# Kernel tuning notes

Measured on AMD Instinct MI355X. Metric: run time of the kernel, lower is better.

Reference implementation:

```python
import jax, jax.numpy as jnp
import numpy as np

T = 4096   # total packed tokens
NQ = 16    # query heads
NK = 4     # kv heads (GQA)
HN = 128   # head dim


def setup_inputs() -> dict:
    key = jax.random.key(0)
    kq, kk, kv = jax.random.split(key, 3)
    return {
        "query": jax.random.normal(kq, (T, NQ, HN), dtype=jnp.float32),
        "key": jax.random.normal(kk, (T, NK, HN), dtype=jnp.float32),
        "value": jax.random.normal(kv, (T, NK, HN), dtype=jnp.float32),
        # packed varlen boundaries (4 sequences)
        "cu_seqlens": jnp.array([0, 1536, 2048, 3584, 4096], dtype=jnp.int32),
    }


def reference(query, key, value, cu_seqlens):
    t, nq, hn = query.shape
    nk = key.shape[1]
    rep = nq // nk  # GQA expansion factor
    scale = hn ** -0.5
    # [h, t, d] layout (matches torch unsqueeze(0).permute(0,2,1,3), batch=1)
    q = jnp.transpose(query, (1, 0, 2))
    k = jnp.repeat(jnp.transpose(key, (1, 0, 2)), rep, axis=0)
    v = jnp.repeat(jnp.transpose(value, (1, 0, 2)), rep, axis=0)
    # full scores [h, t, t]
    scores = jnp.einsum('hqd,hkd->hqk', q, k) * scale
    # block-diagonal causal mask from cu_seqlens
    idx = jnp.arange(t)
    seg = jnp.searchsorted(cu_seqlens[1:], idx, side='right')  # segment id per token
    allowed = (seg[:, None] == seg[None, :]) & (idx[None, :] <= idx[:, None])
    scores = jnp.where(allowed[None, :, :], scores, -jnp.inf)
    p = jax.nn.softmax(scores, axis=-1)  # every row keeps its diagonal -> no NaN
    out = jnp.einsum('hqk,hkd->hqd', p, v)
    # [t, nq*hn]
    return jnp.transpose(out, (1, 0, 2)).reshape(t, nq * hn)
```

## Files before the change

### kernel.cpp

```cpp
#include <hip/hip_runtime.h>
#include <hip/hip_bf16.h>
#include <cstdint>
#include <cstddef>

#define NQH 16
#define NKH 4
#define HN 128
#define QBLK 64
#define KBLK 32
#define QSCALE 0.12751589542585458f

typedef __bf16 bf16x8 __attribute__((ext_vector_type(8)));
typedef float f32x4 __attribute__((ext_vector_type(4)));

__device__ __forceinline__ void gload16(const void* g, void* l) {
  __builtin_amdgcn_global_load_lds(
      (const __attribute__((address_space(1))) void*)g,
      (__attribute__((address_space(3))) void*)l, 16, 0, 0);
}

__global__ __launch_bounds__(256) void cvt_k(const float* __restrict__ K,
                                             __bf16* __restrict__ Kb, int T) {
  const size_t idx8 = ((size_t)blockIdx.x * 256 + threadIdx.x) * 8;
  const int d = (int)(idx8 & 127);
  const int kvh = (int)((idx8 >> 7) & 3);
  const size_t t = idx8 >> 9;
  float4 a = *(const float4*)&K[idx8];
  float4 b = *(const float4*)&K[idx8 + 4];
  bf16x8 f;
  f[0] = (__bf16)a.x; f[1] = (__bf16)a.y; f[2] = (__bf16)a.z; f[3] = (__bf16)a.w;
  f[4] = (__bf16)b.x; f[5] = (__bf16)b.y; f[6] = (__bf16)b.z; f[7] = (__bf16)b.w;
  *(bf16x8*)&Kb[(size_t)kvh * T * HN + t * HN + d] = f;
}

__global__ __launch_bounds__(128) void cvt_v(const float* __restrict__ V,
                                             __bf16* __restrict__ Vb, int T) {
  const int d = threadIdx.x;
  const int t0 = blockIdx.x * 8;
  const int kvh = blockIdx.y;
  bf16x8 f;
#pragma unroll
  for (int i = 0; i < 8; ++i)
    f[i] = (__bf16)V[(size_t)(t0 + i) * (NKH * HN) + kvh * HN + d];
  *(bf16x8*)&Vb[(size_t)kvh * HN * T + (size_t)d * T + t0] = f;
}

template <bool MASKED>
__device__ __forceinline__ void attn_iter(
    const char* Kc, const char* Vc, const bf16x8 qfA[4], const bf16x8 qfB[4],
    int ln, int hi, int vslot, int limA, float& mA, float& lA, f32x4* accA,
    float& mB, float& lB, f32x4* accB) {
  f32x4 sA[2], sB[2];
#pragma unroll
  for (int c = 0; c < 2; ++c) {
    sA[c] = (f32x4){0.f, 0.f, 0.f, 0.f};
    sB[c] = (f32x4){0.f, 0.f, 0.f, 0.f};
  }
  __builtin_amdgcn_s_setprio(1);
#pragma unroll
  for (int kc = 0; kc < 4; ++kc) {
#pragma unroll
    for (int c = 0; c < 2; ++c) {
      const int row = c * 16 + ln;
      const bf16x8 kf =
          *(const bf16x8*)(Kc + row * 256 + (((kc * 4 + hi) ^ (ln & 7)) << 4));
      sA[c] = __builtin_amdgcn_mfma_f32_16x16x32_bf16(kf, qfA[kc], sA[c], 0, 0, 0);
      sB[c] = __builtin_amdgcn_mfma_f32_16x16x32_bf16(kf, qfB[kc], sB[c], 0, 0, 0);
    }
  }
  __builtin_amdgcn_s_setprio(0);

  if (MASKED) {
    const int limB = limA + 16;
#pragma unroll
    for (int c = 0; c < 2; ++c)
#pragma unroll
      for (int i = 0; i < 4; ++i) {
        const int koff = hi * 8 + c * 4 + i;
        sA[c][i] = (koff <= limA) ? sA[c][i] : -1e30f;
        sB[c][i] = (koff <= limB) ? sB[c][i] : -1e30f;
      }
  }

  float mmA = fmaxf(fmaxf(fmaxf(sA[0][0], sA[0][1]), fmaxf(sA[0][2], sA[0][3])),
                    fmaxf(fmaxf(sA[1][0], sA[1][1]), fmaxf(sA[1][2], sA[1][3])));
  float mmB = fmaxf(fmaxf(fmaxf(sB[0][0], sB[0][1]), fmaxf(sB[0][2], sB[0][3])),
                    fmaxf(fmaxf(sB[1][0], sB[1][1]), fmaxf(sB[1][2], sB[1][3])));
  mmA = fmaxf(mmA, __shfl_xor(mmA, 16));
  mmA = fmaxf(mmA, __shfl_xor(mmA, 32));
  mmB = fmaxf(mmB, __shfl_xor(mmB, 16));
  mmB = fmaxf(mmB, __shfl_xor(mmB, 32));

  if (__any((mmA > mA + 8.0f) | (mmB > mB + 8.0f))) {
    const float mnA = fmaxf(mA, mmA), mnB = fmaxf(mB, mmB);
    const float cA = exp2f(mA - mnA), cB = exp2f(mB - mnB);
    mA = mnA; mB = mnB;
    lA *= cA; lB *= cB;
#pragma unroll
    for (int dt = 0; dt < 8; ++dt) { accA[dt] *= cA; accB[dt] *= cB; }
  }

  float pA[2][4], pB[2][4];
  float psA = 0.f, psB = 0.f;
#pragma unroll
  for (int c = 0; c < 2; ++c)
#pragma unroll
    for (int i = 0; i < 4; ++i) {
      pA[c][i] = exp2f(sA[c][i] - mA); psA += pA[c][i];
      pB[c][i] = exp2f(sB[c][i] - mB); psB += pB[c][i];
    }
  psA += __shfl_xor(psA, 16); psA += __shfl_xor(psA, 32);
  psB += __shfl_xor(psB, 16); psB += __shfl_xor(psB, 32);
  lA += psA; lB += psB;

  bf16x8 paA, paB;
#pragma unroll
  for (int e = 0; e < 8; ++e) {
    paA[e] = (__bf16)pA[e >> 2][e & 3];
    paB[e] = (__bf16)pB[e >> 2][e & 3];
  }

  __builtin_amdgcn_s_setprio(1);
#pragma unroll
  for (int dt = 0; dt < 8; ++dt) {
    const int vr = dt * 16 + ln;
    const bf16x8 vb = *(const bf16x8*)(Vc + vr * 64 + vslot);
    accA[dt] = __builtin_amdgcn_mfma_f32_16x16x32_bf16(vb, paA, accA[dt], 0, 0, 0);
    accB[dt] = __builtin_amdgcn_mfma_f32_16x16x32_bf16(vb, paB, accB[dt], 0, 0, 0);
  }
  __builtin_amdgcn_s_setprio(0);
}

__global__ __launch_bounds__(256, 3) void attn_mfma10(
    const float* __restrict__ Q, const __bf16* __restrict__ Kb,
    const __bf16* __restrict__ Vb, const int* __restrict__ cu,
    float* __restrict__ O, int T, int nseg) {
  const int tid = threadIdx.x;
  const int w = tid >> 6, lane = tid & 63;
  const int g = w >> 1, wv = w & 1;
  const int ln = lane & 15, hi = lane >> 4;

  const int bid = blockIdx.x;
  const int round = bid >> 8, pos = bid & 255;
  const int rr = (round & 1) ? ((round << 8) | (255 - pos)) : bid;
  const int h = rr & 15;
  const int my_rank = rr >> 4;
  const int kvh = h >> 2;

  __shared__ __align__(16) char smem[33296];
  float* ml1 = (float*)(smem + 32768);
  int* s_tile = (int*)(smem + 33280);

  if (w == 0) {
    const int t2 = lane;
    const int r0t = t2 << 6;
    int st = 0;
    for (int s = 1; s < nseg; ++s) { const int c = cu[s]; if (c <= r0t) st = c; }
    const int dep = r0t + QBLK - st;
    int rk = 0;
    for (int j = 0; j < 64; ++j) {
      const int dj = __shfl(dep, j);
      rk += (dj > dep) || (dj == dep && j < t2);
    }
    if (rk == my_rank) *s_tile = t2;
  }
  __syncthreads();
  const int r0 = *s_tile << 6;

  int st0 = 0;
  for (int s = 1; s < nseg; ++s) { const int c = cu[s]; if (c <= r0) st0 = c; }
  const int kstart = st0;
  const int n0 = (r0 + QBLK - kstart) >> 6;
  const int gbeg = kstart + g * n0 * KBLK;

  const __bf16* KbH = Kb + (size_t)kvh * T * HN;
  const __bf16* VbH = Vb + (size_t)kvh * HN * T;

  bf16x8 qfA[4], qfB[4];
  {
    const float* qpA = &Q[(size_t)(r0 + wv * 32 + ln) * (NQH * HN) + h * HN];
    const float* qpB = qpA + (size_t)16 * (NQH * HN);
#pragma unroll
    for (int kc = 0; kc < 4; ++kc) {
      float4 a0 = *(const float4*)(qpA + kc * 32 + hi * 8);
      float4 a1 = *(const float4*)(qpA + kc * 32 + hi * 8 + 4);
      float4 b0 = *(const float4*)(qpB + kc * 32 + hi * 8);
      float4 b1 = *(const float4*)(qpB + kc * 32 + hi * 8 + 4);
      bf16x8 fa, fb;
      fa[0] = (__bf16)(a0.x * QSCALE); fa[1] = (__bf16)(a0.y * QSCALE);
      fa[2] = (__bf16)(a0.z * QSCALE); fa[3] = (__bf16)(a0.w * QSCALE);
      fa[4] = (__bf16)(a1.x * QSCALE); fa[5] = (__bf16)(a1.y * QSCALE);
      fa[6] = (__bf16)(a1.z * QSCALE); fa[7] = (__bf16)(a1.w * QSCALE);
      fb[0] = (__bf16)(b0.x * QSCALE); fb[1] = (__bf16)(b0.y * QSCALE);
      fb[2] = (__bf16)(b0.z * QSCALE); fb[3] = (__bf16)(b0.w * QSCALE);
      fb[4] = (__bf16)(b1.x * QSCALE); fb[5] = (__bf16)(b1.y * QSCALE);
      fb[6] = (__bf16)(b1.z * QSCALE); fb[7] = (__bf16)(b1.w * QSCALE);
      qfA[kc] = fa; qfB[kc] = fb;
    }
  }

  float mA = 0.f, lA = 0.f, mB = 0.f, lB = 0.f;
  f32x4 accA[8], accB[8];
#pragma unroll
  for (int dt = 0; dt < 8; ++dt) {
    accA[dt] = (f32x4){0.f, 0.f, 0.f, 0.f};
    accB[dt] = (f32x4){0.f, 0.f, 0.f, 0.f};
  }

  const int gl = wv * 64 + lane;
  const int Rb = gl >> 4, sK = gl & 15;
  int key_j[4];
#pragma unroll
  for (int j = 0; j < 4; ++j)
    key_j[j] = ((Rb >> 2) << 3) + (Rb & 3) + ((j & 1) << 4) + ((j >> 1) << 2);
  const int kcolE = ((sK ^ Rb) << 3);
  const int db = gl >> 2, sV = gl & 3;
  const int swz_d = (db & 3) ^ ((db >> 2) & 3);
  const int vkeyE = ((sV ^ swz_d) << 3);
  char* ldsK = smem + g * 8192 + (size_t)gl * 16;
  char* ldsV = smem + 16384 + g * 8192 + (size_t)gl * 16;
  const int vslot = ((hi ^ (ln & 3) ^ ((ln >> 2) & 3)) << 4);

  const char* Kc = smem + g * 8192;
  const char* Vc = smem + 16384 + g * 8192;
  const int relA = wv * 32 + ln;

  for (int it = 0; it < n0; ++it) {
    const int kb = gbeg + it * KBLK;
#pragma unroll
    for (int j = 0; j < 4; ++j)
      gload16(KbH + (size_t)(kb + key_j[j]) * HN + kcolE, ldsK + j * 2048);
#pragma unroll
    for (int j = 0; j < 4; ++j)
      gload16(VbH + (size_t)(db + 32 * j) * T + kb + vkeyE, ldsV + j * 2048);
    __syncthreads();
    if (kb >= r0)
      attn_iter<true>(Kc, Vc, qfA, qfB, ln, hi, vslot, relA - (kb - r0), mA,
                      lA, accA, mB, lB, accB);
    else
      attn_iter<false>(Kc, Vc, qfA, qfB, ln, hi, vslot, 0, mA, lA, accA, mB,
                       lB, accB);
    __syncthreads();
  }

  float* accf = (float*)smem;
  if (g == 1) {
    if (hi == 0) {
      ml1[relA * 2] = mA;            ml1[relA * 2 + 1] = lA;
      ml1[(relA + 16) * 2] = mB;     ml1[(relA + 16) * 2 + 1] = lB;
    }
#pragma unroll
    for (int dt = 0; dt < 8; ++dt) {
      *(f32x4*)&accf[relA * 128 + ((dt ^ (relA & 7)) << 4) + (hi << 2)] = accA[dt];
      *(f32x4*)&accf[(relA + 16) * 128 + ((dt ^ ((relA + 16) & 7)) << 4) + (hi << 2)] = accB[dt];
    }
  }
  __syncthreads();
  if (g == 0) {
#pragma unroll
    for (int set = 0; set < 2; ++set) {
      const int row = relA + set * 16;
      const float mg = set ? mB : mA;
      const float lg = set ? lB : lA;
      f32x4* acc = set ? accB : accA;
      const float m1 = ml1[row * 2], l1v = ml1[row * 2 + 1];
      float c0 = 1.f, c1 = 0.f, l = lg;
      if (l1v != 0.f) {
        const float m = fmaxf(mg, m1);
        c0 = exp2f(mg - m); c1 = exp2f(m1 - m);
        l = lg * c0 + l1v * c1;
      }
      const float inv = 1.0f / l;
      float* op = &O[(size_t)(r0 + row) * (NQH * HN) + h * HN];
#pragma unroll
      for (int dt = 0; dt < 8; ++dt) {
        const f32x4 a1 = *(const f32x4*)&accf[row * 128 + ((dt ^ (row & 7)) << 4) + (hi << 2)];
        const f32x4 res = (acc[dt] * c0 + a1 * c1) * inv;
        *(f32x4*)&op[dt * 16 + hi * 4] = res;
      }
    }
  }
}

extern "C" void kernel_launch(void* const* d_in, const int* in_sizes, int n_in,
                              void* d_out, int out_size, void* d_ws, size_t ws_size,
                              hipStream_t stream) {
  const float* Q = (const float*)d_in[0];
  const float* K = (const float*)d_in[1];
  const float* V = (const float*)d_in[2];
  const int* cu = (const int*)d_in[3];
  float* O = (float*)d_out;

  const int T = in_sizes[0] / (NQH * HN);
  const int nseg = in_sizes[3] - 1;

  const size_t need = (size_t)2 * NKH * T * HN * sizeof(__bf16);
  if (ws_size < need) return;

  __bf16* Kb = (__bf16*)d_ws;
  __bf16* Vb = (__bf16*)d_ws + (size_t)NKH * T * HN;

  const int nelem = T * NKH * HN;
  cvt_k<<<nelem / 8 / 256, 256, 0, stream>>>(K, Kb, T);
  cvt_v<<<dim3(T / 8, NKH), 128, 0, stream>>>(V, Vb, T);

  attn_mfma10<<<1024, 256, 0, stream>>>(Q, Kb, Vb, cu, O, T, nseg);
}
```

Measured before the change: 72.41 us.

## Load K/V fragments directly from global memory, fuse conversion kernels, defer row-sum reduction

The K and V LDS staging with global_load_lds and the two __syncthreads per iteration are removed, and each lane now reads its bf16 K/V MMA fragments directly from global memory (relying on L1/L2 reuse). The separate K and V conversion kernels are merged into one launch. The per-iteration cross-lane row-sum shuffle is deferred to the end, and the max shuffle now runs only when a rescale is triggered. Occupancy hint drops from 3 to 2 blocks per CU, which trades residency for more registers to hold preloaded fragments, but uncoalesced global fragment loads may expose more latency.

```diff
diff --git a/kernel.cpp b/kernel.cpp
--- a/kernel.cpp
+++ b/kernel.cpp
@@ -13,43 +13,49 @@
 typedef __bf16 bf16x8 __attribute__((ext_vector_type(8)));
 typedef float f32x4 __attribute__((ext_vector_type(4)));
 
-__device__ __forceinline__ void gload16(const void* g, void* l) {
-  __builtin_amdgcn_global_load_lds(
-      (const __attribute__((address_space(1))) void*)g,
-      (__attribute__((address_space(3))) void*)l, 16, 0, 0);
-}
-
-__global__ __launch_bounds__(256) void cvt_k(const float* __restrict__ K,
-                                             __bf16* __restrict__ Kb, int T) {
-  const size_t idx8 = ((size_t)blockIdx.x * 256 + threadIdx.x) * 8;
-  const int d = (int)(idx8 & 127);
-  const int kvh = (int)((idx8 >> 7) & 3);
-  const size_t t = idx8 >> 9;
-  float4 a = *(const float4*)&K[idx8];
-  float4 b = *(const float4*)&K[idx8 + 4];
-  bf16x8 f;
-  f[0] = (__bf16)a.x; f[1] = (__bf16)a.y; f[2] = (__bf16)a.z; f[3] = (__bf16)a.w;
-  f[4] = (__bf16)b.x; f[5] = (__bf16)b.y; f[6] = (__bf16)b.z; f[7] = (__bf16)b.w;
-  *(bf16x8*)&Kb[(size_t)kvh * T * HN + t * HN + d] = f;
-}
-
-__global__ __launch_bounds__(128) void cvt_v(const float* __restrict__ V,
-                                             __bf16* __restrict__ Vb, int T) {
-  const int d = threadIdx.x;
-  const int t0 = blockIdx.x * 8;
-  const int kvh = blockIdx.y;
-  bf16x8 f;
-#pragma unroll
-  for (int i = 0; i < 8; ++i)
-    f[i] = (__bf16)V[(size_t)(t0 + i) * (NKH * HN) + kvh * HN + d];
-  *(bf16x8*)&Vb[(size_t)kvh * HN * T + (size_t)d * T + t0] = f;
+__global__ __launch_bounds__(256) void cvt_kv(const float* __restrict__ K,
+                                              const float* __restrict__ V,
+                                              __bf16* __restrict__ Kb,
+                                              __bf16* __restrict__ Vb, int T) {
+  const int nkblk = T * NKH * HN / 8 / 256;
+  const int bid = blockIdx.x;
+  if (bid < nkblk) {
+    const size_t idx8 = ((size_t)bid * 256 + threadIdx.x) * 8;
+    const int d = (int)(idx8 & 127);
+    const int kvh = (int)((idx8 >> 7) & 3);
+    const size_t t = idx8 >> 9;
+    float4 a = *(const float4*)&K[idx8];
+    float4 b = *(const float4*)&K[idx8 + 4];
+    bf16x8 f;
+    f[0] = (__bf16)a.x; f[1] = (__bf16)a.y; f[2] = (__bf16)a.z; f[3] = (__bf16)a.w;
+    f[4] = (__bf16)b.x; f[5] = (__bf16)b.y; f[6] = (__bf16)b.z; f[7] = (__bf16)b.w;
+    *(bf16x8*)&Kb[(size_t)kvh * T * HN + t * HN + d] = f;
+  } else {
+    const int ob = (bid - nkblk) * 2 + (threadIdx.x >> 7);
+    const int bx = ob & (T / 8 - 1);
+    const int kvh = ob / (T / 8);
+    const int d = threadIdx.x & 127;
+    const int t0 = bx * 8;
+    bf16x8 f;
+#pragma unroll
+    for (int i = 0; i < 8; ++i)
+      f[i] = (__bf16)V[(size_t)(t0 + i) * (NKH * HN) + kvh * HN + d];
+    *(bf16x8*)&Vb[(size_t)kvh * HN * T + (size_t)d * T + t0] = f;
+  }
 }
 
 template <bool MASKED>
 __device__ __forceinline__ void attn_iter(
-    const char* Kc, const char* Vc, const bf16x8 qfA[4], const bf16x8 qfB[4],
-    int ln, int hi, int vslot, int limA, float& mA, float& lA, f32x4* accA,
-    float& mB, float& lB, f32x4* accB) {
+    const __bf16* __restrict__ kA, const __bf16* __restrict__ vA, size_t vstr,
+    const bf16x8 qfA[4], const bf16x8 qfB[4], int hi, int limA,
+    float& mA, float& lA, f32x4* accA, float& mB, float& lB, f32x4* accB) {
+  bf16x8 kf[2][4];
+#pragma unroll
+  for (int c = 0; c < 2; ++c)
+#pragma unroll
+    for (int kc = 0; kc < 4; ++kc)
+      kf[c][kc] = *(const bf16x8*)(kA + c * 4 * HN + kc * 32);
+
   f32x4 sA[2], sB[2];
 #pragma unroll
   for (int c = 0; c < 2; ++c) {
@@ -61,11 +67,8 @@
   for (int kc = 0; kc < 4; ++kc) {
 #pragma unroll
     for (int c = 0; c < 2; ++c) {
-      const int row = c * 16 + ln;
-      const bf16x8 kf =
-          *(const bf16x8*)(Kc + row * 256 + (((kc * 4 + hi) ^ (ln & 7)) << 4));
-      sA[c] = __builtin_amdgcn_mfma_f32_16x16x32_bf16(kf, qfA[kc], sA[c], 0, 0, 0);
-      sB[c] = __builtin_amdgcn_mfma_f32_16x16x32_bf16(kf, qfB[kc], sB[c], 0, 0, 0);
+      sA[c] = __builtin_amdgcn_mfma_f32_16x16x32_bf16(kf[c][kc], qfA[kc], sA[c], 0, 0, 0);
+      sB[c] = __builtin_amdgcn_mfma_f32_16x16x32_bf16(kf[c][kc], qfB[kc], sB[c], 0, 0, 0);
     }
   }
   __builtin_amdgcn_s_setprio(0);
@@ -82,16 +85,15 @@
       }
   }
 
-  float mmA = fmaxf(fmaxf(fmaxf(sA[0][0], sA[0][1]), fmaxf(sA[0][2], sA[0][3])),
-                    fmaxf(fmaxf(sA[1][0], sA[1][1]), fmaxf(sA[1][2], sA[1][3])));
-  float mmB = fmaxf(fmaxf(fmaxf(sB[0][0], sB[0][1]), fmaxf(sB[0][2], sB[0][3])),
-                    fmaxf(fmaxf(sB[1][0], sB[1][1]), fmaxf(sB[1][2], sB[1][3])));
-  mmA = fmaxf(mmA, __shfl_xor(mmA, 16));
-  mmA = fmaxf(mmA, __shfl_xor(mmA, 32));
-  mmB = fmaxf(mmB, __shfl_xor(mmB, 16));
-  mmB = fmaxf(mmB, __shfl_xor(mmB, 32));
-
-  if (__any((mmA > mA + 8.0f) | (mmB > mB + 8.0f))) {
+  const float lmA = fmaxf(fmaxf(fmaxf(sA[0][0], sA[0][1]), fmaxf(sA[0][2], sA[0][3])),
+                          fmaxf(fmaxf(sA[1][0], sA[1][1]), fmaxf(sA[1][2], sA[1][3])));
+  const float lmB = fmaxf(fmaxf(fmaxf(sB[0][0], sB[0][1]), fmaxf(sB[0][2], sB[0][3])),
+                          fmaxf(fmaxf(sB[1][0], sB[1][1]), fmaxf(sB[1][2], sB[1][3])));
+  if (__any((lmA > mA + 8.0f) | (lmB > mB + 8.0f))) {
+    float mmA = fmaxf(lmA, __shfl_xor(lmA, 16));
+    mmA = fmaxf(mmA, __shfl_xor(mmA, 32));
+    float mmB = fmaxf(lmB, __shfl_xor(lmB, 16));
+    mmB = fmaxf(mmB, __shfl_xor(mmB, 32));
     const float mnA = fmaxf(mA, mmA), mnB = fmaxf(mB, mmB);
     const float cA = exp2f(mA - mnA), cB = exp2f(mB - mnB);
     mA = mnA; mB = mnB;
@@ -109,8 +111,6 @@
       pA[c][i] = exp2f(sA[c][i] - mA); psA += pA[c][i];
       pB[c][i] = exp2f(sB[c][i] - mB); psB += pB[c][i];
     }
-  psA += __shfl_xor(psA, 16); psA += __shfl_xor(psA, 32);
-  psB += __shfl_xor(psB, 16); psB += __shfl_xor(psB, 32);
   lA += psA; lB += psB;
 
   bf16x8 paA, paB;
@@ -123,15 +123,14 @@
   __builtin_amdgcn_s_setprio(1);
 #pragma unroll
   for (int dt = 0; dt < 8; ++dt) {
-    const int vr = dt * 16 + ln;
-    const bf16x8 vb = *(const bf16x8*)(Vc + vr * 64 + vslot);
+    const bf16x8 vb = *(const bf16x8*)(vA + (size_t)dt * vstr);
     accA[dt] = __builtin_amdgcn_mfma_f32_16x16x32_bf16(vb, paA, accA[dt], 0, 0, 0);
     accB[dt] = __builtin_amdgcn_mfma_f32_16x16x32_bf16(vb, paB, accB[dt], 0, 0, 0);
   }
   __builtin_amdgcn_s_setprio(0);
 }
 
-__global__ __launch_bounds__(256, 3) void attn_mfma10(
+__global__ __launch_bounds__(256, 2) void attn_reg(
     const float* __restrict__ Q, const __bf16* __restrict__ Kb,
     const __bf16* __restrict__ Vb, const int* __restrict__ cu,
     float* __restrict__ O, int T, int nseg) {
@@ -207,41 +206,26 @@
     accB[dt] = (f32x4){0.f, 0.f, 0.f, 0.f};
   }
 
-  const int gl = wv * 64 + lane;
-  const int Rb = gl >> 4, sK = gl & 15;
-  int key_j[4];
-#pragma unroll
-  for (int j = 0; j < 4; ++j)
-    key_j[j] = ((Rb >> 2) << 3) + (Rb & 3) + ((j & 1) << 4) + ((j >> 1) << 2);
-  const int kcolE = ((sK ^ Rb) << 3);
-  const int db = gl >> 2, sV = gl & 3;
-  const int swz_d = (db & 3) ^ ((db >> 2) & 3);
-  const int vkeyE = ((sV ^ swz_d) << 3);
-  char* ldsK = smem + g * 8192 + (size_t)gl * 16;
-  char* ldsV = smem + 16384 + g * 8192 + (size_t)gl * 16;
-  const int vslot = ((hi ^ (ln & 3) ^ ((ln >> 2) & 3)) << 4);
-
-  const char* Kc = smem + g * 8192;
-  const char* Vc = smem + 16384 + g * 8192;
+  const int krow = ((ln >> 2) << 3) + (ln & 3);
+  const __bf16* kA = KbH + (size_t)(gbeg + krow) * HN + hi * 8;
+  const __bf16* vA = VbH + (size_t)ln * T + gbeg + hi * 8;
+  const size_t vstr = (size_t)16 * T;
   const int relA = wv * 32 + ln;
 
   for (int it = 0; it < n0; ++it) {
     const int kb = gbeg + it * KBLK;
-#pragma unroll
-    for (int j = 0; j < 4; ++j)
-      gload16(KbH + (size_t)(kb + key_j[j]) * HN + kcolE, ldsK + j * 2048);
-#pragma unroll
-    for (int j = 0; j < 4; ++j)
-      gload16(VbH + (size_t)(db + 32 * j) * T + kb + vkeyE, ldsV + j * 2048);
-    __syncthreads();
     if (kb >= r0)
-      attn_iter<true>(Kc, Vc, qfA, qfB, ln, hi, vslot, relA - (kb - r0), mA,
-                      lA, accA, mB, lB, accB);
+      attn_iter<true>(kA, vA, vstr, qfA, qfB, hi, relA - (kb - r0), mA, lA,
+                      accA, mB, lB, accB);
     else
-      attn_iter<false>(Kc, Vc, qfA, qfB, ln, hi, vslot, 0, mA, lA, accA, mB,
-                       lB, accB);
-    __syncthreads();
-  }
+      attn_iter<false>(kA, vA, vstr, qfA, qfB, hi, 0, mA, lA, accA, mB, lB,
+                       accB);
+    kA += (size_t)KBLK * HN;
+    vA += KBLK;
+  }
+
+  lA += __shfl_xor(lA, 16); lA += __shfl_xor(lA, 32);
+  lB += __shfl_xor(lB, 16); lB += __shfl_xor(lB, 32);
 
   float* accf = (float*)smem;
   if (g == 1) {
@@ -300,9 +284,8 @@
   __bf16* Kb = (__bf16*)d_ws;
   __bf16* Vb = (__bf16*)d_ws + (size_t)NKH * T * HN;
 
-  const int nelem = T * NKH * HN;
-  cvt_k<<<nelem / 8 / 256, 256, 0, stream>>>(K, Kb, T);
-  cvt_v<<<dim3(T / 8, NKH), 128, 0, stream>>>(V, Vb, T);
-
-  attn_mfma10<<<1024, 256, 0, stream>>>(Q, Kb, Vb, cu, O, T, nseg);
-}
+  const int nkblk = T * NKH * HN / 8 / 256;
+  cvt_kv<<<2 * nkblk, 256, 0, stream>>>(K, V, Kb, Vb, T);
+
+  attn_reg<<<1024, 256, 0, stream>>>(Q, Kb, Vb, cu, O, T, nseg);
+}
```

New measurement: 117.0 us. 61.6% more time.
